# Kernel optimization log

Hardware: AMD Instinct MI355X
Metric: run time of the kernel (lower is better)

## Reference

```python
import jax, jax.numpy as jnp
import numpy as np

B, T, D = 64, 128, 1024
E = 2048      # embedding_dim of state encoder
CD = 256      # VQ code_dim
NC = 1024     # num_codes
BETA = 0.25   # commitment cost


def setup_inputs() -> dict:
    key = jax.random.key(0)
    ks = jax.random.split(key, 5)
    states = jax.random.normal(ks[0], (B, T, D), dtype=jnp.float32)
    next_states = jax.random.normal(ks[1], (B, T, D), dtype=jnp.float32)
    # VarianceScaling(scale=2.0, fan_in) init
    W_s = jax.random.normal(ks[2], (D, E), dtype=jnp.float32) * np.sqrt(2.0 / D)
    b_s = jnp.zeros((E,), dtype=jnp.float32)
    W_p = jax.random.normal(ks[3], (2 * E, CD), dtype=jnp.float32) * np.sqrt(2.0 / (2 * E))
    b_p = jnp.zeros((CD,), dtype=jnp.float32)
    codebook = jax.random.normal(ks[4], (NC, CD), dtype=jnp.float32)
    return {"states": states, "next_states": next_states, "W_s": W_s,
            "b_s": b_s, "W_p": W_p, "b_p": b_p, "codebook": codebook}


def reference(states, next_states, W_s, b_s, W_p, b_p, codebook):
    # dual state encoder (shared weights)
    se = states @ W_s + b_s            # (B,T,E)
    ne = next_states @ W_s + b_s       # (B,T,E)
    policy_input = jax.nn.gelu(jnp.concatenate([se, ne], axis=-1))  # (B,T,2E)
    latent = policy_input @ W_p + b_p  # (B,T,CD)

    # --- VectorQuantizerEMA forward ---
    flat = latent.reshape(-1, CD)      # (N, CD), N = B*T
    # squared euclidean distances to codebook rows
    dists = (jnp.sum(flat * flat, axis=1, keepdims=True)
             - 2.0 * flat @ codebook.T
             + jnp.sum(codebook * codebook, axis=1))  # (N, NC)
    idx = jnp.argmin(dists, axis=1)                    # (N,)
    encodings = jax.nn.one_hot(idx, NC, dtype=latent.dtype)  # (N, NC)
    quantize = codebook[idx].reshape(latent.shape)     # (B,T,CD)

    e_latent_loss = jnp.mean(jnp.square(jax.lax.stop_gradient(quantize) - latent))
    loss = BETA * e_latent_loss
    # straight-through estimator
    quantize_st = latent + jax.lax.stop_gradient(quantize - latent)

    avg_probs = jnp.mean(encodings, axis=0)
    perplexity = jnp.exp(-jnp.sum(avg_probs * jnp.log(avg_probs + 1e-10)))

    encodings = encodings.reshape(B, T, NC)
    encoding_indices = idx.reshape(B, T)
    return quantize_st, loss, perplexity, encodings, encoding_indices
```

## Files before the change

### kernel.cpp

```cpp
#include <hip/hip_runtime.h>

#define NROW  8192
#define D_    1024
#define E_    2048
#define P2E_  4096
#define CD_   256
#define NC_   1024
#define BETA_ 0.25f
#define SPLITK 8

typedef __attribute__((ext_vector_type(8))) short short8;
typedef __attribute__((ext_vector_type(4))) float f32x4;

__device__ __forceinline__ ushort f2bf(float x) {
    union { float f; unsigned u; } v; v.f = x;
    unsigned r = (v.u + 0x7fffu + ((v.u >> 16) & 1u)) >> 16;
    return (ushort)r;
}
__device__ __forceinline__ float bf2f(ushort h) {
    union { unsigned u; float f; } v; v.u = ((unsigned)h) << 16;
    return v.f;
}
__device__ __forceinline__ void split2(float x, ushort& h, ushort& l) {
    h = f2bf(x);
    l = f2bf(x - bf2f(h));
}
__device__ __forceinline__ float gelu_tanh(float x) {
    float x3 = x * x * x;
    return 0.5f * x * (1.0f + tanhf(0.7978845608028654f * (x + 0.044715f * x3)));
}

#define GLD16(gp, lp) __builtin_amdgcn_global_load_lds( \
    (const __attribute__((address_space(1))) void*)(gp), \
    (__attribute__((address_space(3))) void*)(lp), 16, 0, 0)

template<int EPI>
__global__ __launch_bounds__(256)
void gemm_bf16x3(const ushort* __restrict__ Ah, const ushort* __restrict__ Al,
                 const ushort* __restrict__ Bh, const ushort* __restrict__ Bl,
                 int K, int ksteps,
                 const float* __restrict__ bias,
                 float* __restrict__ outF,
                 ushort* __restrict__ oPh, ushort* __restrict__ oPl,
                 const float* __restrict__ cn,
                 float* __restrict__ candv, int* __restrict__ candi)
{
    __shared__ alignas(16) ushort sAh[2][4096], sAl[2][4096], sBh[2][4096], sBl[2][4096];
    __shared__ float redv[128][2];
    __shared__ int   redi[128][2];
    const int t = threadIdx.x;
    const int l = t & 63;
    const int w = t >> 6;
    const int wr = w >> 1, wc = w & 1;

    const int nxy = gridDim.x * gridDim.y;
    const int id  = blockIdx.y * gridDim.x + blockIdx.x;
    const int swz = (id & 7) * (nxy >> 3) + (id >> 3);
    const int bx  = swz % gridDim.x;
    const int by  = swz / gridDim.x;

    const int bm = by * 128;
    const int bn = bx * 128;
    const int kstart = (EPI == 1) ? (int)blockIdx.z * (ksteps * 32) : 0;

    const int srow = t >> 2;
    const int scol = ((t & 3) ^ ((t >> 3) & 3)) * 8;
    const ushort* gAh = Ah + (size_t)(bm + srow) * K + kstart + scol;
    const ushort* gAl = Al + (size_t)(bm + srow) * K + kstart + scol;
    const ushort* gBh = Bh + (size_t)(bn + srow) * K + kstart + scol;
    const ushort* gBl = Bl + (size_t)(bn + srow) * K + kstart + scol;
    const size_t rstep = (size_t)64 * K;
    const int lo0 = t * 8, lo1 = t * 8 + 2048;

    f32x4 acc[4][4];
#pragma unroll
    for (int i = 0; i < 4; i++)
#pragma unroll
        for (int j = 0; j < 4; j++) acc[i][j] = (f32x4)0.0f;

    const int rsw = ((l >> 4) ^ (((l & 15) >> 1) & 3)) * 8;
    const int ar = (wr * 64 + (l & 15)) * 32 + rsw;
    const int br = (wc * 64 + (l & 15)) * 32 + rsw;

#define STAGE8(b) do { \
        GLD16(gAh, &sAh[b][lo0]); GLD16(gAh + rstep, &sAh[b][lo1]); \
        GLD16(gAl, &sAl[b][lo0]); GLD16(gAl + rstep, &sAl[b][lo1]); \
        GLD16(gBh, &sBh[b][lo0]); GLD16(gBh + rstep, &sBh[b][lo1]); \
        GLD16(gBl, &sBl[b][lo0]); GLD16(gBl + rstep, &sBl[b][lo1]); \
    } while (0)

    STAGE8(0);
    __syncthreads();

    for (int s = 0; s < ksteps; ++s) {
        const int cb_ = s & 1;
        if (s + 1 < ksteps) {
            gAh += 32; gAl += 32; gBh += 32; gBl += 32;
            STAGE8(cb_ ^ 1);
        }
        short8 fah[4], fal[4], fbh[4], fbl[4];
#pragma unroll
        for (int i = 0; i < 4; i++) {
            fah[i] = *(const short8*)&sAh[cb_][ar + i * 16 * 32];
            fal[i] = *(const short8*)&sAl[cb_][ar + i * 16 * 32];
            fbh[i] = *(const short8*)&sBh[cb_][br + i * 16 * 32];
            fbl[i] = *(const short8*)&sBl[cb_][br + i * 16 * 32];
        }
        __builtin_amdgcn_s_setprio(1);
#pragma unroll
        for (int i = 0; i < 4; i++)
#pragma unroll
            for (int j = 0; j < 4; j++) {
                acc[i][j] = __builtin_amdgcn_mfma_f32_16x16x32_bf16(fah[i], fbh[j], acc[i][j], 0, 0, 0);
                acc[i][j] = __builtin_amdgcn_mfma_f32_16x16x32_bf16(fah[i], fbl[j], acc[i][j], 0, 0, 0);
                acc[i][j] = __builtin_amdgcn_mfma_f32_16x16x32_bf16(fal[i], fbh[j], acc[i][j], 0, 0, 0);
            }
        __builtin_amdgcn_s_setprio(0);
        __syncthreads();
    }
#undef STAGE8

    if constexpr (EPI == 2) {
        float cnv[4];
#pragma unroll
        for (int j = 0; j < 4; j++) cnv[j] = cn[bn + wc * 64 + j * 16 + (l & 15)];
#pragma unroll
        for (int i = 0; i < 4; i++) {
            const int grow = bm + wr * 64 + i * 16 + (l >> 4) * 4;
#pragma unroll
            for (int r = 0; r < 4; r++) {
                float bv = INFINITY; int bi = 0;
#pragma unroll
                for (int j = 0; j < 4; j++) {
                    float d = cnv[j] - 2.0f * acc[i][j][r];
                    int c = bn + wc * 64 + j * 16 + (l & 15);
                    if (d < bv) { bv = d; bi = c; }
                }
#pragma unroll
                for (int m = 1; m < 16; m <<= 1) {
                    float ov = __shfl_xor(bv, m, 64);
                    int   oi = __shfl_xor(bi, m, 64);
                    if (ov < bv || (ov == bv && oi < bi)) { bv = ov; bi = oi; }
                }
                int rl = wr * 64 + i * 16 + (l >> 4) * 4 + r;
                if ((l & 15) == 0) { redv[rl][wc] = bv; redi[rl][wc] = bi; }
#pragma unroll
                for (int j = 0; j < 4; j++)
                    outF[(size_t)(grow + r) * NC_ + bn + wc * 64 + j * 16 + (l & 15)] = 0.0f;
            }
        }
        __syncthreads();
        if (t < 128) {
            float v0 = redv[t][0], v1 = redv[t][1];
            int   i0 = redi[t][0], i1 = redi[t][1];
            bool take1 = (v1 < v0) || (v1 == v0 && i1 < i0);
            candv[(size_t)(bm + t) * 8 + bx] = take1 ? v1 : v0;
            candi[(size_t)(bm + t) * 8 + bx] = take1 ? i1 : i0;
        }
        return;
    }

#pragma unroll
    for (int i = 0; i < 4; i++) {
        const int grow = bm + wr * 64 + i * 16 + (l >> 4) * 4;
#pragma unroll
        for (int j = 0; j < 4; j++) {
            const int gcol = bn + wc * 64 + j * 16 + (l & 15);
            f32x4 a = acc[i][j];
            if constexpr (EPI == 0) {
                const float bb = bias[gcol];
#pragma unroll
                for (int r = 0; r < 4; r++) {
                    int m = grow + r;
                    float x = gelu_tanh(a[r] + bb);
                    ushort h, lo; split2(x, h, lo);
                    int pr = (m < NROW) ? m : m - NROW;
                    int pc = ((m < NROW) ? 0 : E_) + gcol;
                    oPh[(size_t)pr * P2E_ + pc] = h;
                    oPl[(size_t)pr * P2E_ + pc] = lo;
                }
            } else if constexpr (EPI == 1) {
                float* o = outF + ((size_t)NROW * blockIdx.z + grow) * CD_ + gcol;
#pragma unroll
                for (int r = 0; r < 4; r++) o[(size_t)r * CD_] = a[r];
            }
        }
    }
}

__global__ void split_k(const float* __restrict__ in, ushort* __restrict__ oh,
                        ushort* __restrict__ ol, int n4)
{
    int i = blockIdx.x * blockDim.x + threadIdx.x;
    int stride = gridDim.x * blockDim.x;
    for (; i < n4; i += stride) {
        float4 v = ((const float4*)in)[i];
        ushort4 h, lo;
        split2(v.x, h.x, lo.x); split2(v.y, h.y, lo.y);
        split2(v.z, h.z, lo.z); split2(v.w, h.w, lo.w);
        ((ushort4*)oh)[i] = h;
        ((ushort4*)ol)[i] = lo;
    }
}

__global__ __launch_bounds__(1024)
void tsplit_k(const float* __restrict__ in, ushort* __restrict__ oh,
              ushort* __restrict__ ol, int R, int C)
{
    __shared__ float tile[32][33];
    int c0 = blockIdx.x * 32, r0 = blockIdx.y * 32;
    int tx = threadIdx.x, ty = threadIdx.y;
    tile[ty][tx] = in[(size_t)(r0 + ty) * C + c0 + tx];
    __syncthreads();
    float x = tile[tx][ty];
    ushort h, lo; split2(x, h, lo);
    size_t o = (size_t)(c0 + ty) * R + r0 + tx;
    oh[o] = h; ol[o] = lo;
}

__global__ __launch_bounds__(256)
void combine_k(const float* __restrict__ part, const float* __restrict__ bias,
               float* __restrict__ latent, ushort* __restrict__ lh,
               ushort* __restrict__ ll)
{
    int row = blockIdx.x, t = threadIdx.x;
    float x = bias[t];
#pragma unroll
    for (int z = 0; z < SPLITK; z++) x += part[((size_t)z * NROW + row) * CD_ + t];
    latent[(size_t)row * CD_ + t] = x;
    ushort h, lo; split2(x, h, lo);
    lh[(size_t)row * CD_ + t] = h;
    ll[(size_t)row * CD_ + t] = lo;
}

__global__ __launch_bounds__(256) void row_norms(const float* __restrict__ X,
                                                 float* __restrict__ out)
{
    __shared__ float s[256];
    int n = blockIdx.x, t = threadIdx.x;
    float v = X[(size_t)n * 256 + t];
    s[t] = v * v;
    __syncthreads();
    for (int st = 128; st > 0; st >>= 1) {
        if (t < st) s[t] += s[t + st];
        __syncthreads();
    }
    if (t == 0) out[n] = s[0];
}

__global__ void zero_hist(int* hist) { hist[threadIdx.x] = 0; }

__global__ __launch_bounds__(256) void vq2_kernel(
    const float* __restrict__ latent, const float* __restrict__ cb,
    const float* __restrict__ candv, const int* __restrict__ candi,
    float* __restrict__ out_enc, float* __restrict__ out_q,
    float* __restrict__ out_idx, int* __restrict__ hist, float* __restrict__ lpart)
{
    __shared__ float sd[256];
    __shared__ int sbc;
    const int n = blockIdx.x, t = threadIdx.x;
    if (t == 0) {
        const float* cv = candv + (size_t)n * 8;
        const int*   ci = candi + (size_t)n * 8;
        float bv = cv[0]; int bi = ci[0];
#pragma unroll
        for (int k = 1; k < 8; k++) {
            float v = cv[k]; int x = ci[k];
            if (v < bv || (v == bv && x < bi)) { bv = v; bi = x; }
        }
        sbc = bi;
    }
    __syncthreads();
    const int bc = sbc;
    if (t == 0) out_enc[(size_t)n * NC_ + bc] = 1.0f;

    float lv = latent[(size_t)n * CD_ + t];
    float q  = cb[(size_t)bc * CD_ + t];
    out_q[(size_t)n * CD_ + t] = lv + (q - lv);
    float diff = q - lv;
    sd[t] = diff * diff;
    __syncthreads();
    for (int st = 128; st > 0; st >>= 1) {
        if (t < st) sd[t] += sd[t + st];
        __syncthreads();
    }
    if (t == 0) {
        lpart[n] = sd[0];
        atomicAdd(&hist[bc], 1);
        out_idx[n] = (float)bc;
    }
}

__global__ __launch_bounds__(1024) void finalize_kernel(
    const float* __restrict__ lpart, const int* __restrict__ hist,
    float* __restrict__ out_loss, float* __restrict__ out_perp)
{
    __shared__ float s[1024];
    int t = threadIdx.x;
    float x = 0.0f;
    for (int i = t; i < NROW; i += 1024) x += lpart[i];
    s[t] = x;
    __syncthreads();
    for (int st = 512; st > 0; st >>= 1) {
        if (t < st) s[t] += s[t + st];
        __syncthreads();
    }
    float total = s[0];
    __syncthreads();
    float p = (float)hist[t] * (1.0f / NROW);
    s[t] = p * logf(p + 1e-10f);
    __syncthreads();
    for (int st = 512; st > 0; st >>= 1) {
        if (t < st) s[t] += s[t + st];
        __syncthreads();
    }
    if (t == 0) {
        *out_loss = BETA_ * (total / (float)((size_t)NROW * CD_));
        *out_perp = expf(-s[0]);
    }
}

extern "C" void kernel_launch(void* const* d_in, const int* in_sizes, int n_in,
                              void* d_out, int out_size, void* d_ws, size_t ws_size,
                              hipStream_t stream)
{
    const float* states      = (const float*)d_in[0];
    const float* next_states = (const float*)d_in[1];
    const float* W_s         = (const float*)d_in[2];
    const float* b_s         = (const float*)d_in[3];
    const float* W_p         = (const float*)d_in[4];
    const float* b_p         = (const float*)d_in[5];
    const float* codebook    = (const float*)d_in[6];

    float* out      = (float*)d_out;
    float* out_q    = out;
    float* out_loss = out + (size_t)NROW * CD_;
    float* out_perp = out_loss + 1;
    float* out_enc  = out_perp + 1;
    float* out_idx  = out_enc + (size_t)NROW * NC_;

    char* ws = (char*)d_ws;
    size_t off = 0;
    auto alloc = [&](size_t bytes) { void* p = ws + off; off += (bytes + 255) & ~255ull; return p; };

    ushort* A1h  = (ushort*)alloc((size_t)2 * NROW * D_ * 2);
    ushort* A1l  = (ushort*)alloc((size_t)2 * NROW * D_ * 2);
    ushort* WsTh = (ushort*)alloc((size_t)E_ * D_ * 2);
    ushort* WsTl = (ushort*)alloc((size_t)E_ * D_ * 2);
    ushort* WpTh = (ushort*)alloc((size_t)CD_ * P2E_ * 2);
    ushort* WpTl = (ushort*)alloc((size_t)CD_ * P2E_ * 2);
    ushort* cbh  = (ushort*)alloc((size_t)NC_ * CD_ * 2);
    ushort* cbl  = (ushort*)alloc((size_t)NC_ * CD_ * 2);
    ushort* Ph   = (ushort*)alloc((size_t)NROW * P2E_ * 2);
    ushort* Pl   = (ushort*)alloc((size_t)NROW * P2E_ * 2);
    ushort* lath = (ushort*)alloc((size_t)NROW * CD_ * 2);
    ushort* latl = (ushort*)alloc((size_t)NROW * CD_ * 2);
    float*  cbn  = (float*)alloc(NC_ * 4);
    int*    hist = (int*)alloc(NC_ * 4);
    float*  lpart= (float*)alloc(NROW * 4);
    float*  candv= (float*)alloc((size_t)NROW * 8 * 4);
    int*    candi= (int*)alloc((size_t)NROW * 8 * 4);
    float* lat_part = (float*)A1h;
    float* latent   = (float*)WsTh;

    {
        int n4 = NROW * D_ / 4;
        split_k<<<2048, 256, 0, stream>>>(states, A1h, A1l, n4);
        split_k<<<2048, 256, 0, stream>>>(next_states, A1h + (size_t)NROW * D_,
                                          A1l + (size_t)NROW * D_, n4);
    }
    tsplit_k<<<dim3(E_ / 32, D_ / 32), dim3(32, 32), 0, stream>>>(W_s, WsTh, WsTl, D_, E_);
    tsplit_k<<<dim3(CD_ / 32, P2E_ / 32), dim3(32, 32), 0, stream>>>(W_p, WpTh, WpTl, P2E_, CD_);
    split_k<<<256, 256, 0, stream>>>(codebook, cbh, cbl, NC_ * CD_ / 4);
    row_norms<<<NC_, 256, 0, stream>>>(codebook, cbn);

    gemm_bf16x3<0><<<dim3(E_ / 128, 2 * NROW / 128), 256, 0, stream>>>(
        A1h, A1l, WsTh, WsTl, D_, D_ / 32, b_s, nullptr, Ph, Pl, nullptr, nullptr, nullptr);

    gemm_bf16x3<1><<<dim3(CD_ / 128, NROW / 128, SPLITK), 256, 0, stream>>>(
        Ph, Pl, WpTh, WpTl, P2E_, P2E_ / 32 / SPLITK, nullptr, lat_part, nullptr, nullptr,
        nullptr, nullptr, nullptr);

    combine_k<<<NROW, 256, 0, stream>>>(lat_part, b_p, latent, lath, latl);

    gemm_bf16x3<2><<<dim3(NC_ / 128, NROW / 128), 256, 0, stream>>>(
        lath, latl, cbh, cbl, CD_, CD_ / 32, nullptr, out_enc, nullptr, nullptr,
        cbn, candv, candi);

    zero_hist<<<1, NC_, 0, stream>>>(hist);
    vq2_kernel<<<NROW, 256, 0, stream>>>(latent, codebook, candv, candi,
                                         out_enc, out_q, out_idx, hist, lpart);
    finalize_kernel<<<1, 1024, 0, stream>>>(lpart, hist, out_loss, out_perp);
}
```

Measured before the change: 378.8 us.

## Switch GEMM to single-buffered LDS and alias reduction scratch to tile buffers

Replaces the double-buffered LDS tiles with a single buffer. Each k-step now reads its fragments into registers, synchronizes, and then issues the next global-to-LDS loads before running the MFMAs. The epilogue's argmin reduction arrays now reuse the tile buffers instead of separate shared arrays. Halving LDS use (64KB down to about 32KB) is meant to let more blocks fit per CU, but it gives up overlap between loads and the previous tile's LDS reads and adds a barrier per step.

Result: faster. 359.2 us (-5.2%).

```diff
diff --git a/kernel.cpp b/kernel.cpp
--- a/kernel.cpp
+++ b/kernel.cpp
@@ -45,9 +45,7 @@
                  const float* __restrict__ cn,
                  float* __restrict__ candv, int* __restrict__ candi)
 {
-    __shared__ alignas(16) ushort sAh[2][4096], sAl[2][4096], sBh[2][4096], sBl[2][4096];
-    __shared__ float redv[128][2];
-    __shared__ int   redi[128][2];
+    __shared__ alignas(16) ushort sAh[4096], sAl[4096], sBh[4096], sBl[4096];
     const int t = threadIdx.x;
     const int l = t & 63;
     const int w = t >> 6;
@@ -82,30 +80,32 @@
     const int ar = (wr * 64 + (l & 15)) * 32 + rsw;
     const int br = (wc * 64 + (l & 15)) * 32 + rsw;
 
-#define STAGE8(b) do { \
-        GLD16(gAh, &sAh[b][lo0]); GLD16(gAh + rstep, &sAh[b][lo1]); \
-        GLD16(gAl, &sAl[b][lo0]); GLD16(gAl + rstep, &sAl[b][lo1]); \
-        GLD16(gBh, &sBh[b][lo0]); GLD16(gBh + rstep, &sBh[b][lo1]); \
-        GLD16(gBl, &sBl[b][lo0]); GLD16(gBl + rstep, &sBl[b][lo1]); \
+#define STAGE8() do { \
+        GLD16(gAh, &sAh[lo0]); GLD16(gAh + rstep, &sAh[lo1]); \
+        GLD16(gAl, &sAl[lo0]); GLD16(gAl + rstep, &sAl[lo1]); \
+        GLD16(gBh, &sBh[lo0]); GLD16(gBh + rstep, &sBh[lo1]); \
+        GLD16(gBl, &sBl[lo0]); GLD16(gBl + rstep, &sBl[lo1]); \
     } while (0)
 
-    STAGE8(0);
+    STAGE8();
     __syncthreads();
 
     for (int s = 0; s < ksteps; ++s) {
-        const int cb_ = s & 1;
+        short8 fah[4], fal[4], fbh[4], fbl[4];
+#pragma unroll
+        for (int i = 0; i < 4; i++) {
+            fah[i] = *(const short8*)&sAh[ar + i * 16 * 32];
+            fal[i] = *(const short8*)&sAl[ar + i * 16 * 32];
+            fbh[i] = *(const short8*)&sBh[br + i * 16 * 32];
+            fbl[i] = *(const short8*)&sBl[br + i * 16 * 32];
+        }
+        __syncthreads();
+
         if (s + 1 < ksteps) {
             gAh += 32; gAl += 32; gBh += 32; gBl += 32;
-            STAGE8(cb_ ^ 1);
-        }
-        short8 fah[4], fal[4], fbh[4], fbl[4];
-#pragma unroll
-        for (int i = 0; i < 4; i++) {
-            fah[i] = *(const short8*)&sAh[cb_][ar + i * 16 * 32];
-            fal[i] = *(const short8*)&sAl[cb_][ar + i * 16 * 32];
-            fbh[i] = *(const short8*)&sBh[cb_][br + i * 16 * 32];
-            fbl[i] = *(const short8*)&sBl[cb_][br + i * 16 * 32];
-        }
+            STAGE8();
+        }
+
         __builtin_amdgcn_s_setprio(1);
 #pragma unroll
         for (int i = 0; i < 4; i++)
@@ -121,6 +121,8 @@
 #undef STAGE8
 
     if constexpr (EPI == 2) {
+        float (*redv)[2] = (float(*)[2])sAh;
+        int   (*redi)[2] = (int(*)[2])sAl;
         float cnv[4];
 #pragma unroll
         for (int j = 0; j < 4; j++) cnv[j] = cn[bn + wc * 64 + j * 16 + (l & 15)];
```
